# Kernel tuning notes

Measured on AMD Instinct MI355X. Metric: run time of the kernel, lower is better.

The kernel has to match this reference:

```python
import jax, jax.numpy as jnp
import numpy as np

B, S, D, DO = 4, 2048, 1024, 1024
E, K = 20, 2  # num_experts = 4*4 + 4, top-k = 2


def setup_inputs() -> dict:
    key = jax.random.key(0)
    ks = jax.random.split(key, 6)
    sc_d = 1.0 / np.sqrt(D)
    sc_h = 1.0 / np.sqrt(D // 4)
    return {
        "x": jax.random.normal(ks[0], (B, S, D), jnp.float32),
        "wg1": jax.random.normal(ks[1], (D, D // 4), jnp.float32) * sc_d,
        "bg1": jnp.zeros((D // 4,), jnp.float32),
        "wg2": jax.random.normal(ks[2], (D // 4, 2 * E), jnp.float32) * sc_h,
        "bg2": jnp.zeros((2 * E,), jnp.float32),
        "We": jax.random.normal(ks[3], (E, D, DO), jnp.float32) * sc_d,
        "be": jnp.zeros((E, DO), jnp.float32),
    }


def reference(x, wg1, bg1, wg2, bg2, We, be):
    Bv, Sv, Dv = x.shape
    xf = x.reshape(-1, Dv)                                 # [N, D] flattened tokens
    # gating MLP: Linear -> GELU (exact, erf) -> Linear, output 2*E wide
    h = jax.nn.gelu(xf @ wg1 + bg1, approximate=False)
    logits = (xf @ 0.0 + (h @ wg2 + bg2))[:, :E] if False else (h @ wg2 + bg2)[:, :E]  # chunk(2)[0]: clean logits (eval, no noise)
    probs = jax.nn.softmax(logits, axis=-1)                # [N, E]
    top_vals, top_idx = jax.lax.top_k(probs, K)            # [N, K]
    N = xf.shape[0]
    # dense gate matrix = zeros.scatter(1, top_k_indices, top_k_gates)
    gates = jnp.zeros((N, E), xf.dtype).at[jnp.arange(N)[:, None], top_idx].set(top_vals)
    # combine: y = sum_e gates[:, e] * (x @ W_e + b_e)  (same math as dispatch/expert/scatter-add)
    def body(y, eb):
        We_e, be_e, g_e = eb
        return y + g_e[:, None] * (xf @ We_e + be_e), None
    y0 = jnp.zeros((N, be.shape[-1]), xf.dtype)
    y, _ = jax.lax.scan(body, y0, (We, be, gates.T))
    return y.reshape(Bv, Sv, -1)
```

## Files before the change

kernel.cpp:

```cpp
#include <hip/hip_runtime.h>
#include <hip/hip_bf16.h>
#include <math.h>


#define N_TOK 8192
#define DIM   1024
#define DHID  256
#define DOUT  1024
#define NE    20
#define BM2   128
#define BN2   128
#define BK2   64
#define MAX_TT 148

typedef __attribute__((ext_vector_type(8))) short bf16x8;
typedef __attribute__((ext_vector_type(4))) float f32x4;

__device__ __forceinline__ float gelu_erf(float v) {
    return 0.5f * v * (1.0f + erff(v * 0.70710678118654752f));
}

__device__ __forceinline__ ushort f2b(float f) {
  union { float f; uint u; } c; c.f = f;
  uint r = (c.u + 0x7FFFu + ((c.u >> 16) & 1u)) >> 16;
  return (ushort)r;
}

__device__ __forceinline__ float b2f(ushort u) {
  union { uint u; float f; } c; c.u = ((uint)u) << 16;
  return c.f;
}

__global__ __launch_bounds__(256) void k_front(
    const float* __restrict__ x, const float* __restrict__ wg1,
    const float* __restrict__ bg1, float* __restrict__ h,
    const float* __restrict__ We, ushort* __restrict__ weT,
    ushort* __restrict__ xb) {
  __shared__ __align__(1024) char smem[17408];
  const int bid = blockIdx.x;
  const int t = threadIdx.x;

  if (bid < 512) {
    char* XsB = smem;
    char* WsB = smem + 8192;
    float (*Ws)[64] = (float(*)[64])WsB;
    const int ty = t >> 4, tx = t & 15;
    const int m0 = (bid >> 2) * 64;
    const int c0 = (bid & 3) * 64;

    const float* xsrc[2];
    char* xdst[2];
    const float* wsrc[2];
    char* wdst[2];
#pragma unroll
    for (int l = 0; l < 2; ++l) {
      int i = t + l * 256;
      int row = i >> 3, seg = i & 7;
      xsrc[l] = x + (size_t)(m0 + row) * DIM + ((seg ^ ((row >> 2) & 7)) << 2);
      xdst[l] = XsB + i * 16;
      int kk = i >> 4, sg2 = i & 15;
      wsrc[l] = wg1 + (size_t)kk * DHID + c0 + sg2 * 4;
      wdst[l] = WsB + i * 16;
    }

    float acc[4][4] = {};
    for (int k0 = 0; k0 < DIM; k0 += 32) {
#pragma unroll
      for (int l = 0; l < 2; ++l)
        __builtin_amdgcn_global_load_lds(xsrc[l] + k0, (float*)xdst[l], 16, 0, 0);
#pragma unroll
      for (int l = 0; l < 2; ++l)
        __builtin_amdgcn_global_load_lds(wsrc[l] + (size_t)k0 * DHID, (float*)wdst[l], 16, 0, 0);
      __syncthreads();
#pragma unroll
      for (int q = 0; q < 8; ++q) {
        float4 a[4];
        const int qs = (q ^ (ty & 7)) << 4;
#pragma unroll
        for (int i = 0; i < 4; ++i)
          a[i] = *(const float4*)(XsB + (ty * 4 + i) * 128 + qs);
#pragma unroll
        for (int u = 0; u < 4; ++u) {
          float4 b = *(const float4*)&Ws[q * 4 + u][tx * 4];
#pragma unroll
          for (int i = 0; i < 4; ++i) {
            float av = reinterpret_cast<const float*>(&a[i])[u];
            acc[i][0] += av * b.x;
            acc[i][1] += av * b.y;
            acc[i][2] += av * b.z;
            acc[i][3] += av * b.w;
          }
        }
      }
      __syncthreads();
    }
#pragma unroll
    for (int i = 0; i < 4; ++i) {
      int row = m0 + ty * 4 + i;
      int col = c0 + tx * 4;
      float4 o;
      o.x = gelu_erf(acc[i][0] + bg1[col + 0]);
      o.y = gelu_erf(acc[i][1] + bg1[col + 1]);
      o.z = gelu_erf(acc[i][2] + bg1[col + 2]);
      o.w = gelu_erf(acc[i][3] + bg1[col + 3]);
      *(float4*)&h[(size_t)row * DHID + col] = o;
    }
  } else if (bid < 5632) {
    ushort* Ts = (ushort*)smem;
    const int b = bid - 512;
    const int e = b >> 8, rem = b & 255;
    const int k0 = (rem >> 4) * 64;
    const int n0 = (rem & 15) * 64;
    const float* src = We + ((size_t)e << 20);
    const int m = t & 15;
    const int xk = (m & 7) << 3;
#pragma unroll
    for (int it = 0; it < 4; ++it) {
      int kk = it * 16 + (t >> 4);
      int nn = m * 4;
      float4 v = *(const float4*)(src + (size_t)(k0 + kk) * DOUT + n0 + nn);
      int col = kk ^ xk;
      Ts[(nn + 0) * 64 + col] = f2b(v.x);
      Ts[(nn + 1) * 64 + col] = f2b(v.y);
      Ts[(nn + 2) * 64 + col] = f2b(v.z);
      Ts[(nn + 3) * 64 + col] = f2b(v.w);
    }
    __syncthreads();
    ushort* dst = weT + ((size_t)e << 20);
#pragma unroll
    for (int it = 0; it < 2; ++it) {
      int nn = it * 32 + (t >> 3);
      int ks = (t & 7) * 8;
      int cs = ks ^ (((nn >> 2) & 7) << 3);
      uint4 v = *(const uint4*)&Ts[nn * 64 + cs];
      *(uint4*)(dst + (size_t)(n0 + nn) * DIM + k0 + ks) = v;
    }
  } else {
    const size_t i0 = (((size_t)(bid - 5632)) * 256 + t) * 16;
    ushort o[16];
#pragma unroll
    for (int j = 0; j < 4; ++j) {
      float4 v = *(const float4*)(x + i0 + j * 4);
      o[j * 4 + 0] = f2b(v.x); o[j * 4 + 1] = f2b(v.y);
      o[j * 4 + 2] = f2b(v.z); o[j * 4 + 3] = f2b(v.w);
    }
    *(uint4*)(xb + i0)     = *(const uint4*)&o[0];
    *(uint4*)(xb + i0 + 8) = *(const uint4*)&o[8];
  }
}

__global__ __launch_bounds__(64) void k_router(
    const float* __restrict__ h, const float* __restrict__ wg2,
    const float* __restrict__ bg2, int* __restrict__ tokexp,
    float* __restrict__ tokgate, int* __restrict__ counts) {
  __shared__ float swg[DHID * NE];
  __shared__ int hist[NE];
  const int t = threadIdx.x;
  if (t < NE) hist[t] = 0;
  for (int i = t; i < DHID * NE; i += 64) {
    int k = i / NE, j = i - k * NE;
    swg[i] = wg2[(size_t)k * (2 * NE) + j];
  }
  __syncthreads();
  const int n = blockIdx.x * 64 + t;
  float s[NE];
#pragma unroll
  for (int j = 0; j < NE; ++j) s[j] = bg2[j];
  const float* hr = h + (size_t)n * DHID;
  for (int k = 0; k < DHID; k += 4) {
    float4 hv = *(const float4*)(hr + k);
#pragma unroll
    for (int u = 0; u < 4; ++u) {
      float hvu = reinterpret_cast<const float*>(&hv)[u];
      const float4* wrow = (const float4*)&swg[(k + u) * NE];
      float wl[NE];
      *(float4*)&wl[0]  = wrow[0];
      *(float4*)&wl[4]  = wrow[1];
      *(float4*)&wl[8]  = wrow[2];
      *(float4*)&wl[12] = wrow[3];
      *(float4*)&wl[16] = wrow[4];
#pragma unroll
      for (int j = 0; j < NE; ++j) s[j] += hvu * wl[j];
    }
  }
  float m = s[0];
#pragma unroll
  for (int j = 1; j < NE; ++j) m = fmaxf(m, s[j]);
  float sum = 0.0f;
#pragma unroll
  for (int j = 0; j < NE; ++j) { s[j] = expf(s[j] - m); sum += s[j]; }
  float inv = 1.0f / sum;
#pragma unroll
  for (int j = 0; j < NE; ++j) s[j] *= inv;
  int j0 = 0; float v0 = s[0];
#pragma unroll
  for (int j = 1; j < NE; ++j) if (s[j] > v0) { v0 = s[j]; j0 = j; }
  int j1 = -1; float v1 = -1.0f;
#pragma unroll
  for (int j = 0; j < NE; ++j)
    if (j != j0 && s[j] > v1) { v1 = s[j]; j1 = j; }
  tokexp[2 * n + 0] = j0;  tokgate[2 * n + 0] = v0;
  tokexp[2 * n + 1] = j1;  tokgate[2 * n + 1] = v1;
  atomicAdd(&hist[j0], 1);
  atomicAdd(&hist[j1], 1);
  __syncthreads();
  if (t < NE) atomicAdd(&counts[t], hist[t]);
}

__global__ __launch_bounds__(256) void k_scatter(
    const int* __restrict__ tokexp, const float* __restrict__ tokgate,
    const int* __restrict__ counts, int* __restrict__ zcur,
    int* __restrict__ perm, float* __restrict__ pgate, int* __restrict__ inv) {
  __shared__ int soff[NE], lcnt[NE], lbase[NE];
  const int t = threadIdx.x;
  if (t < NE) lcnt[t] = 0;
  if (t < 64) {
    int c = (t < NE) ? counts[t] : 0;
    int cs = c;
    for (int d = 1; d < 64; d <<= 1) {
      int u = __shfl_up(cs, d); if (t >= d) cs += u;
    }
    if (t < NE) soff[t] = cs - c;
  }
  __syncthreads();
  const int n = blockIdx.x * 256 + t;
  const int e0 = tokexp[2 * n + 0];
  const int e1 = tokexp[2 * n + 1];
  const int r0 = atomicAdd(&lcnt[e0], 1);
  const int r1 = atomicAdd(&lcnt[e1], 1);
  __syncthreads();
  if (t < NE) lbase[t] = atomicAdd(&zcur[t], lcnt[t]);
  __syncthreads();
  {
    int pos = soff[e0] + lbase[e0] + r0;
    perm[pos] = n;
    pgate[pos] = tokgate[2 * n + 0];
    inv[2 * n + 0] = pos;
  }
  {
    int pos = soff[e1] + lbase[e1] + r1;
    perm[pos] = n;
    pgate[pos] = tokgate[2 * n + 1];
    inv[2 * n + 1] = pos;
  }
}

__global__ __launch_bounds__(256) void k_expert(
    const ushort* __restrict__ xb, const ushort* __restrict__ weT,
    const float* __restrict__ be, const int* __restrict__ perm,
    const float* __restrict__ pgate, const int* __restrict__ counts,
    ushort* __restrict__ contrib) {
  const int lin = blockIdx.x + blockIdx.y * MAX_TT;
  const int nt8 = (lin & 7) * MAX_TT + (lin >> 3);
  const int rt = nt8 >> 3, pn = nt8 & 7;

  __shared__ __align__(1024) char smem[66560];
  int*    stok  = (int*)smem;
  float*  sgate = (float*)(smem + 512);
  ushort* As0   = (ushort*)(smem + 1024);
  ushort* Bs0   = (ushort*)(smem + 17408);
  __shared__ int tinfo[3];

  const int t = threadIdx.x;
  if (t < 64) {
    if (t == 0) tinfo[0] = -1;
    int c = (t < NE) ? counts[t] : 0;
    int nt = (c + BM2 - 1) >> 7;
    int cs = c, ts = nt;
    for (int d = 1; d < 64; d <<= 1) {
      int u = __shfl_up(cs, d); if (t >= d) cs += u;
      int v = __shfl_up(ts, d); if (t >= d) ts += v;
    }
    int coff = cs - c, toff = ts - nt;
    if (t < NE && rt >= toff && rt < toff + nt) {
      int i = rt - toff;
      tinfo[0] = t;
      tinfo[1] = coff + i * BM2;
      tinfo[2] = min(BM2, c - i * BM2);
    }
  }
  __syncthreads();
  if (tinfo[0] < 0) return;
  const int e = tinfo[0], rs = tinfo[1], cnt = tinfo[2];
  const int c0 = pn * BN2;

  if (t < BM2) {
    int r = (t < cnt) ? rs + t : rs;
    stok[t]  = perm[r];
    sgate[t] = (t < cnt) ? pgate[rs + t] : 0.0f;
  }
  __syncthreads();
  const int lane = t & 63, w = t >> 6;
  const int wr = w >> 1, wc = w & 1;
  const int lr = lane & 15, hi = lane >> 4;
  const int srow = lane >> 3, sseg = lane & 7;

  const ushort* asrc[4];
  const ushort* bsrc[4];
  ushort* adst[4];
  ushort* bdst[4];
#pragma unroll
  for (int l = 0; l < 4; ++l) {
    int r = w * 32 + l * 8 + srow;
    asrc[l] = xb + (size_t)stok[r] * DIM + ((sseg ^ (r & 7)) << 3);
    adst[l] = As0 + (w * 32 + l * 8) * BK2;
    bsrc[l] = weT + ((size_t)e << 20) + (size_t)(c0 + r) * DIM + ((sseg ^ (r & 7)) << 3);
    bdst[l] = Bs0 + (w * 32 + l * 8) * BK2;
  }

  f32x4 acc[4][4] = {};

#pragma unroll
  for (int l = 0; l < 4; ++l)
    __builtin_amdgcn_global_load_lds(asrc[l], adst[l], 16, 0, 0);
#pragma unroll
  for (int l = 0; l < 4; ++l)
    __builtin_amdgcn_global_load_lds(bsrc[l], bdst[l], 16, 0, 0);

  int cur = 0;
  for (int k0 = 0; k0 < DIM; k0 += BK2) {
    __syncthreads();
    const int nxt = cur ^ 1;
    if (k0 + BK2 < DIM) {
      const int koff = k0 + BK2;
      const int dsh = nxt ? 16384 : 0;
#pragma unroll
      for (int l = 0; l < 4; ++l)
        __builtin_amdgcn_global_load_lds(asrc[l] + koff, adst[l] + dsh, 16, 0, 0);
#pragma unroll
      for (int l = 0; l < 4; ++l)
        __builtin_amdgcn_global_load_lds(bsrc[l] + koff, bdst[l] + dsh, 16, 0, 0);
    }
    const char* Ab = (const char*)smem + 1024 + (cur ? 32768 : 0);
    const char* Bb = Ab + 16384;
#pragma unroll
    for (int ks = 0; ks < 2; ++ks) {
      const int kb = ks * 64 + hi * 16;
      bf16x8 af[4], bfr[4];
#pragma unroll
      for (int mi = 0; mi < 4; ++mi) {
        int r = wr * 64 + mi * 16 + lr;
        af[mi] = *(const bf16x8*)(Ab + r * 128 + (kb ^ ((r & 7) << 4)));
      }
#pragma unroll
      for (int ni = 0; ni < 4; ++ni) {
        int n = wc * 64 + ni * 16 + lr;
        bfr[ni] = *(const bf16x8*)(Bb + n * 128 + (kb ^ ((n & 7) << 4)));
      }
#pragma unroll
      for (int mi = 0; mi < 4; ++mi)
#pragma unroll
        for (int ni = 0; ni < 4; ++ni)
          acc[mi][ni] = __builtin_amdgcn_mfma_f32_16x16x32_bf16(
              af[mi], bfr[ni], acc[mi][ni], 0, 0, 0);
    }
    cur = nxt;
  }
  __syncthreads();

  ushort (*Ep)[72] = (ushort(*)[72])(smem + 1024 + w * 9216);
  float bcol[4];
#pragma unroll
  for (int ni = 0; ni < 4; ++ni)
    bcol[ni] = be[(size_t)e * DOUT + c0 + wc * 64 + ni * 16 + lr];
#pragma unroll
  for (int mi = 0; mi < 4; ++mi)
#pragma unroll
    for (int r = 0; r < 4; ++r) {
      int rowl = mi * 16 + hi * 4 + r;
      float g = sgate[wr * 64 + rowl];
#pragma unroll
      for (int ni = 0; ni < 4; ++ni)
        Ep[rowl][ni * 16 + lr] = f2b(g * (acc[mi][ni][r] + bcol[ni]));
    }
  __syncthreads();
#pragma unroll
  for (int it = 0; it < 8; ++it) {
    int rowl = it * 8 + (lane >> 3);
    int slotL = wr * 64 + rowl;
    if (slotL < cnt) {
      uint4 v = *(const uint4*)&Ep[rowl][(lane & 7) * 8];
      *(uint4*)(contrib + (size_t)(rs + slotL) * DOUT + c0 + wc * 64 + (lane & 7) * 8) = v;
    }
  }
}

__global__ __launch_bounds__(256) void k_reduce(
    const ushort* __restrict__ contrib, const int* __restrict__ inv,
    float* __restrict__ y) {
  const int t = threadIdx.x;
  const int n = blockIdx.x * 2 + (t >> 7);
  const int c = (t & 127) * 8;
  const int p0 = inv[2 * n], p1 = inv[2 * n + 1];
  uint4 a = *(const uint4*)(contrib + (size_t)p0 * DOUT + c);
  uint4 b = *(const uint4*)(contrib + (size_t)p1 * DOUT + c);
  const ushort* ua = (const ushort*)&a;
  const ushort* ub = (const ushort*)&b;
  float4 o0, o1;
  o0.x = b2f(ua[0]) + b2f(ub[0]);
  o0.y = b2f(ua[1]) + b2f(ub[1]);
  o0.z = b2f(ua[2]) + b2f(ub[2]);
  o0.w = b2f(ua[3]) + b2f(ub[3]);
  o1.x = b2f(ua[4]) + b2f(ub[4]);
  o1.y = b2f(ua[5]) + b2f(ub[5]);
  o1.z = b2f(ua[6]) + b2f(ub[6]);
  o1.w = b2f(ua[7]) + b2f(ub[7]);
  float* yr = y + (size_t)n * DOUT + c;
  *(float4*)yr = o0;
  *(float4*)(yr + 4) = o1;
}

extern "C" void kernel_launch(void* const* d_in, const int* in_sizes, int n_in,
                              void* d_out, int out_size, void* d_ws, size_t ws_size,
                              hipStream_t stream) {
  (void)in_sizes; (void)n_in; (void)ws_size; (void)out_size;
  const float* x   = (const float*)d_in[0];
  const float* wg1 = (const float*)d_in[1];
  const float* bg1 = (const float*)d_in[2];
  const float* wg2 = (const float*)d_in[3];
  const float* bg2 = (const float*)d_in[4];
  const float* We  = (const float*)d_in[5];
  const float* be  = (const float*)d_in[6];
  float* y = (float*)d_out;

  char* ws = (char*)d_ws;
  float*  h       = (float*)ws;
  ushort* xb      = (ushort*)(ws + (size_t)N_TOK * DHID * 4);
  ushort* weT     = (ushort*)((char*)xb + (size_t)N_TOK * DIM * 2);
  ushort* contrib = (ushort*)((char*)weT + (size_t)NE * DIM * DOUT * 2);
  char*   ctrl    = (char*)contrib + (size_t)2 * N_TOK * DOUT * 2;
  int*   counts  = (int*)ctrl;
  int*   zcur    = counts + 64;
  int*   tokexp  = counts + 128;
  float* tokgate = (float*)(tokexp + 2 * N_TOK);
  int*   perm    = (int*)(tokgate + 2 * N_TOK);
  float* pgate   = (float*)(perm + 2 * N_TOK);
  int*   inv     = (int*)(pgate + 2 * N_TOK);

  hipMemsetAsync(counts, 0, 128 * sizeof(int), stream);

  k_front<<<dim3(512 + 5120 + 2048), 256, 0, stream>>>(x, wg1, bg1, h, We, weT, xb);
  k_router<<<dim3(N_TOK / 64), 64, 0, stream>>>(h, wg2, bg2, tokexp, tokgate, counts);
  k_scatter<<<dim3(N_TOK / 256), 256, 0, stream>>>(tokexp, tokgate, counts, zcur,
                                                   perm, pgate, inv);
  k_expert<<<dim3(MAX_TT, DOUT / BN2), 256, 0, stream>>>(
      xb, weT, be, perm, pgate, counts, contrib);
  k_reduce<<<dim3(N_TOK / 2), 256, 0, stream>>>(contrib, inv, y);
}
```

Measured before the change: 186.3 us.

## Compute gating GEMM with split-bf16 MFMA and fold counts reset into front kernel

The fp32 FMA gating GEMM inside the front kernel is replaced by a separate kernel using bf16 MFMA with a hi/lo split of x and wg1. Three MFMAs per tile approximate fp32 accuracy. The front kernel now also emits the low-part bf16 of x, transposes and splits wg1, and zeroes the counts buffer, which removes the memset call. In exchange it adds an extra launch and extra traffic for the xlo arrays, and the routing precision changes slightly.

```diff
diff --git a/kernel.cpp b/kernel.cpp
--- a/kernel.cpp
+++ b/kernel.cpp
@@ -33,81 +33,17 @@
 
 __global__ __launch_bounds__(256) void k_front(
     const float* __restrict__ x, const float* __restrict__ wg1,
-    const float* __restrict__ bg1, float* __restrict__ h,
     const float* __restrict__ We, ushort* __restrict__ weT,
-    ushort* __restrict__ xb) {
-  __shared__ __align__(1024) char smem[17408];
+    ushort* __restrict__ xb, ushort* __restrict__ xlo,
+    ushort* __restrict__ w1h, ushort* __restrict__ w1l,
+    int* __restrict__ counts) {
+  __shared__ __align__(1024) char smem[16384];
   const int bid = blockIdx.x;
   const int t = threadIdx.x;
 
-  if (bid < 512) {
-    char* XsB = smem;
-    char* WsB = smem + 8192;
-    float (*Ws)[64] = (float(*)[64])WsB;
-    const int ty = t >> 4, tx = t & 15;
-    const int m0 = (bid >> 2) * 64;
-    const int c0 = (bid & 3) * 64;
-
-    const float* xsrc[2];
-    char* xdst[2];
-    const float* wsrc[2];
-    char* wdst[2];
-#pragma unroll
-    for (int l = 0; l < 2; ++l) {
-      int i = t + l * 256;
-      int row = i >> 3, seg = i & 7;
-      xsrc[l] = x + (size_t)(m0 + row) * DIM + ((seg ^ ((row >> 2) & 7)) << 2);
-      xdst[l] = XsB + i * 16;
-      int kk = i >> 4, sg2 = i & 15;
-      wsrc[l] = wg1 + (size_t)kk * DHID + c0 + sg2 * 4;
-      wdst[l] = WsB + i * 16;
-    }
-
-    float acc[4][4] = {};
-    for (int k0 = 0; k0 < DIM; k0 += 32) {
-#pragma unroll
-      for (int l = 0; l < 2; ++l)
-        __builtin_amdgcn_global_load_lds(xsrc[l] + k0, (float*)xdst[l], 16, 0, 0);
-#pragma unroll
-      for (int l = 0; l < 2; ++l)
-        __builtin_amdgcn_global_load_lds(wsrc[l] + (size_t)k0 * DHID, (float*)wdst[l], 16, 0, 0);
-      __syncthreads();
-#pragma unroll
-      for (int q = 0; q < 8; ++q) {
-        float4 a[4];
-        const int qs = (q ^ (ty & 7)) << 4;
-#pragma unroll
-        for (int i = 0; i < 4; ++i)
-          a[i] = *(const float4*)(XsB + (ty * 4 + i) * 128 + qs);
-#pragma unroll
-        for (int u = 0; u < 4; ++u) {
-          float4 b = *(const float4*)&Ws[q * 4 + u][tx * 4];
-#pragma unroll
-          for (int i = 0; i < 4; ++i) {
-            float av = reinterpret_cast<const float*>(&a[i])[u];
-            acc[i][0] += av * b.x;
-            acc[i][1] += av * b.y;
-            acc[i][2] += av * b.z;
-            acc[i][3] += av * b.w;
-          }
-        }
-      }
-      __syncthreads();
-    }
-#pragma unroll
-    for (int i = 0; i < 4; ++i) {
-      int row = m0 + ty * 4 + i;
-      int col = c0 + tx * 4;
-      float4 o;
-      o.x = gelu_erf(acc[i][0] + bg1[col + 0]);
-      o.y = gelu_erf(acc[i][1] + bg1[col + 1]);
-      o.z = gelu_erf(acc[i][2] + bg1[col + 2]);
-      o.w = gelu_erf(acc[i][3] + bg1[col + 3]);
-      *(float4*)&h[(size_t)row * DHID + col] = o;
-    }
-  } else if (bid < 5632) {
+  if (bid < 5120) {
     ushort* Ts = (ushort*)smem;
-    const int b = bid - 512;
+    const int b = bid;
     const int e = b >> 8, rem = b & 255;
     const int k0 = (rem >> 4) * 64;
     const int n0 = (rem & 15) * 64;
@@ -135,18 +71,160 @@
       uint4 v = *(const uint4*)&Ts[nn * 64 + cs];
       *(uint4*)(dst + (size_t)(n0 + nn) * DIM + k0 + ks) = v;
     }
-  } else {
-    const size_t i0 = (((size_t)(bid - 5632)) * 256 + t) * 16;
-    ushort o[16];
+  } else if (bid < 7168) {
+    if (bid == 7167 && t < 128) counts[t] = 0;
+    const size_t i0 = (((size_t)(bid - 5120)) * 256 + t) * 16;
+    ushort oh[16], ol[16];
 #pragma unroll
     for (int j = 0; j < 4; ++j) {
       float4 v = *(const float4*)(x + i0 + j * 4);
-      o[j * 4 + 0] = f2b(v.x); o[j * 4 + 1] = f2b(v.y);
-      o[j * 4 + 2] = f2b(v.z); o[j * 4 + 3] = f2b(v.w);
-    }
-    *(uint4*)(xb + i0)     = *(const uint4*)&o[0];
-    *(uint4*)(xb + i0 + 8) = *(const uint4*)&o[8];
-  }
+      const float* vf = (const float*)&v;
+#pragma unroll
+      for (int u = 0; u < 4; ++u) {
+        ushort hu = f2b(vf[u]);
+        oh[j * 4 + u] = hu;
+        ol[j * 4 + u] = f2b(vf[u] - b2f(hu));
+      }
+    }
+    *(uint4*)(xb + i0)      = *(const uint4*)&oh[0];
+    *(uint4*)(xb + i0 + 8)  = *(const uint4*)&oh[8];
+    *(uint4*)(xlo + i0)     = *(const uint4*)&ol[0];
+    *(uint4*)(xlo + i0 + 8) = *(const uint4*)&ol[8];
+  } else {
+    ushort* Th = (ushort*)smem;
+    ushort* Tl = (ushort*)(smem + 8192);
+    const int b2 = bid - 7168;
+    const int k0 = (b2 >> 2) * 64;
+    const int n0 = (b2 & 3) * 64;
+    const int m = t & 15;
+    const int xk = (m & 7) << 3;
+#pragma unroll
+    for (int it = 0; it < 4; ++it) {
+      int kk = it * 16 + (t >> 4);
+      int nn = m * 4;
+      float4 v = *(const float4*)(wg1 + (size_t)(k0 + kk) * DHID + n0 + nn);
+      const float* vf = (const float*)&v;
+      int col = kk ^ xk;
+#pragma unroll
+      for (int u = 0; u < 4; ++u) {
+        ushort hu = f2b(vf[u]);
+        Th[(nn + u) * 64 + col] = hu;
+        Tl[(nn + u) * 64 + col] = f2b(vf[u] - b2f(hu));
+      }
+    }
+    __syncthreads();
+#pragma unroll
+    for (int it = 0; it < 2; ++it) {
+      int nn = it * 32 + (t >> 3);
+      int ks = (t & 7) * 8;
+      int cs = ks ^ (((nn >> 2) & 7) << 3);
+      uint4 vh = *(const uint4*)&Th[nn * 64 + cs];
+      uint4 vl = *(const uint4*)&Tl[nn * 64 + cs];
+      *(uint4*)(w1h + (size_t)(n0 + nn) * DIM + k0 + ks) = vh;
+      *(uint4*)(w1l + (size_t)(n0 + nn) * DIM + k0 + ks) = vl;
+    }
+  }
+}
+
+__global__ __launch_bounds__(256) void k_gate(
+    const ushort* __restrict__ xb, const ushort* __restrict__ xlo,
+    const ushort* __restrict__ w1h, const ushort* __restrict__ w1l,
+    const float* __restrict__ bg1, float* __restrict__ h) {
+  __shared__ __align__(1024) char smem[65536];
+  const int t = threadIdx.x;
+  const int m0 = blockIdx.x * 64;
+  const int c0 = blockIdx.y * 64;
+  const int lane = t & 63, w = t >> 6;
+  const int wr = w >> 1, wc = w & 1;
+  const int lr = lane & 15, hi = lane >> 4;
+
+  const ushort* gsrc[8];
+  ushort* gdst[8];
+  {
+    const ushort* mats[4] = {xb, xlo, w1h, w1l};
+#pragma unroll
+    for (int m = 0; m < 4; ++m) {
+      int rbase = (m < 2) ? m0 : c0;
+#pragma unroll
+      for (int l = 0; l < 2; ++l) {
+        int i = t + l * 256;
+        int row = i >> 3, seg = i & 7;
+        gsrc[m * 2 + l] = mats[m] + (size_t)(rbase + row) * DIM +
+                          ((seg ^ (row & 7)) << 3);
+        gdst[m * 2 + l] = (ushort*)smem + m * 4096 + i * 8;
+      }
+    }
+  }
+
+  f32x4 acc[2][2] = {};
+
+#pragma unroll
+  for (int j = 0; j < 8; ++j)
+    __builtin_amdgcn_global_load_lds(gsrc[j], gdst[j], 16, 0, 0);
+
+  int cur = 0;
+  for (int k0 = 0; k0 < DIM; k0 += 64) {
+    __syncthreads();
+    if (k0 + 64 < DIM) {
+      const int koff = k0 + 64;
+      const int dsh = (cur ^ 1) ? 16384 : 0;
+#pragma unroll
+      for (int j = 0; j < 8; ++j)
+        __builtin_amdgcn_global_load_lds(gsrc[j] + koff, gdst[j] + dsh, 16, 0, 0);
+    }
+    const char* base = smem + (cur ? 32768 : 0);
+    const char* Ah = base;
+    const char* Al = base + 8192;
+    const char* Bh = base + 16384;
+    const char* Bl = base + 24576;
+#pragma unroll
+    for (int ks = 0; ks < 2; ++ks) {
+      const int kb = ks * 64 + hi * 16;
+      bf16x8 ah[2], al[2], bh[2], bl[2];
+#pragma unroll
+      for (int mi = 0; mi < 2; ++mi) {
+        int r = wr * 32 + mi * 16 + lr;
+        int off = r * 128 + (kb ^ ((r & 7) << 4));
+        ah[mi] = *(const bf16x8*)(Ah + off);
+        al[mi] = *(const bf16x8*)(Al + off);
+      }
+#pragma unroll
+      for (int ni = 0; ni < 2; ++ni) {
+        int n = wc * 32 + ni * 16 + lr;
+        int off = n * 128 + (kb ^ ((n & 7) << 4));
+        bh[ni] = *(const bf16x8*)(Bh + off);
+        bl[ni] = *(const bf16x8*)(Bl + off);
+      }
+#pragma unroll
+      for (int mi = 0; mi < 2; ++mi)
+#pragma unroll
+        for (int ni = 0; ni < 2; ++ni) {
+          acc[mi][ni] = __builtin_amdgcn_mfma_f32_16x16x32_bf16(
+              ah[mi], bh[ni], acc[mi][ni], 0, 0, 0);
+          acc[mi][ni] = __builtin_amdgcn_mfma_f32_16x16x32_bf16(
+              ah[mi], bl[ni], acc[mi][ni], 0, 0, 0);
+          acc[mi][ni] = __builtin_amdgcn_mfma_f32_16x16x32_bf16(
+              al[mi], bh[ni], acc[mi][ni], 0, 0, 0);
+        }
+    }
+    cur ^= 1;
+  }
+
+  float bcol[2];
+#pragma unroll
+  for (int ni = 0; ni < 2; ++ni)
+    bcol[ni] = bg1[c0 + wc * 32 + ni * 16 + lr];
+#pragma unroll
+  for (int mi = 0; mi < 2; ++mi)
+#pragma unroll
+    for (int r = 0; r < 4; ++r) {
+      int row = m0 + wr * 32 + mi * 16 + hi * 4 + r;
+#pragma unroll
+      for (int ni = 0; ni < 2; ++ni) {
+        int col = c0 + wc * 32 + ni * 16 + lr;
+        h[(size_t)row * DHID + col] = gelu_erf(acc[mi][ni][r] + bcol[ni]);
+      }
+    }
 }
 
 __global__ __launch_bounds__(64) void k_router(
@@ -426,8 +504,11 @@
   char* ws = (char*)d_ws;
   float*  h       = (float*)ws;
   ushort* xb      = (ushort*)(ws + (size_t)N_TOK * DHID * 4);
-  ushort* weT     = (ushort*)((char*)xb + (size_t)N_TOK * DIM * 2);
-  ushort* contrib = (ushort*)((char*)weT + (size_t)NE * DIM * DOUT * 2);
+  ushort* xlo     = (ushort*)((char*)xb + (size_t)N_TOK * DIM * 2);
+  ushort* weT     = (ushort*)((char*)xlo + (size_t)N_TOK * DIM * 2);
+  ushort* w1h     = (ushort*)((char*)weT + (size_t)NE * DIM * DOUT * 2);
+  ushort* w1l     = w1h + (size_t)DHID * DIM;
+  ushort* contrib = w1l + (size_t)DHID * DIM;
   char*   ctrl    = (char*)contrib + (size_t)2 * N_TOK * DOUT * 2;
   int*   counts  = (int*)ctrl;
   int*   zcur    = counts + 64;
@@ -437,9 +518,10 @@
   float* pgate   = (float*)(perm + 2 * N_TOK);
   int*   inv     = (int*)(pgate + 2 * N_TOK);
 
-  hipMemsetAsync(counts, 0, 128 * sizeof(int), stream);
-
-  k_front<<<dim3(512 + 5120 + 2048), 256, 0, stream>>>(x, wg1, bg1, h, We, weT, xb);
+  k_front<<<dim3(5120 + 2048 + 64), 256, 0, stream>>>(
+      x, wg1, We, weT, xb, xlo, w1h, w1l, counts);
+  k_gate<<<dim3(N_TOK / 64, DHID / 64), 256, 0, stream>>>(
+      xb, xlo, w1h, w1l, bg1, h);
   k_router<<<dim3(N_TOK / 64), 64, 0, stream>>>(h, wg2, bg2, tokexp, tokgate, counts);
   k_scatter<<<dim3(N_TOK / 256), 256, 0, stream>>>(tokexp, tokgate, counts, zcur,
                                                    perm, pgate, inv);
```

After: 151.3 us (median of 2 runs). -18.8%, faster.
